# Optimization experiments

Hardware: AMD Instinct MI355X
Metric: run time of the kernel (lower is better)

## Reference

```python
import jax, jax.numpy as jnp
import numpy as np

S, B, D, H, L = 512, 1, 1024, 1024, 2  # seq, batch(=1 forced by view([1,-1])), input, hidden, layers


def _lstm_scan(xs, w_ih, w_hh, b, reverse=False):
    """Run an LSTMCell over xs [S,1,in]; returns (h_final, c_final, outs [S,1,H]).
    Torch LSTMCell gate order: i, f, g, o. b = b_ih + b_hh (combined)."""
    Hd = w_hh.shape[1]
    def step(carry, x):
        h, c = carry
        gates = x @ w_ih.T + h @ w_hh.T + b  # [1, 4H]
        i, f, g, o = jnp.split(gates, 4, axis=-1)
        c = jax.nn.sigmoid(f) * c + jax.nn.sigmoid(i) * jnp.tanh(g)
        h = jax.nn.sigmoid(o) * jnp.tanh(c)
        return (h, c), h
    init = (jnp.zeros((1, Hd), xs.dtype), jnp.zeros((1, Hd), xs.dtype))
    (h, c), outs = jax.lax.scan(step, init, xs, reverse=reverse)
    return h, c, outs


def setup_inputs() -> dict:
    key = jax.random.key(0)
    ks = jax.random.split(key, 13)
    sc = lambda fan_in: 1.0 / np.sqrt(fan_in)
    def W(k, rows, cols):
        return jax.random.uniform(k, (rows, cols), jnp.float32, -sc(cols), sc(cols))
    inp = {"x": jax.random.normal(ks[0], (S, B, D), jnp.float32)}
    # layer 0 (input D), fwd and bwd cells
    inp["w_ih0f"] = W(ks[1], 4 * H, D); inp["w_hh0f"] = W(ks[2], 4 * H, H)
    inp["b0f"] = jnp.zeros((4 * H,), jnp.float32)
    inp["w_ih0b"] = W(ks[3], 4 * H, D); inp["w_hh0b"] = W(ks[4], 4 * H, H)
    inp["b0b"] = jnp.zeros((4 * H,), jnp.float32)
    # layer 1 (input 2H from bidirectional concat)
    inp["w_ih1f"] = W(ks[5], 4 * H, 2 * H); inp["w_hh1f"] = W(ks[6], 4 * H, H)
    inp["b1f"] = jnp.zeros((4 * H,), jnp.float32)
    inp["w_ih1b"] = W(ks[7], 4 * H, 2 * H); inp["w_hh1b"] = W(ks[8], 4 * H, H)
    inp["b1b"] = jnp.zeros((4 * H,), jnp.float32)
    return inp


def reference(x, w_ih0f, w_hh0f, b0f, w_ih0b, w_hh0b, b0b,
              w_ih1f, w_hh1f, b1f, w_ih1b, w_hh1b, b1b):
    xs = x.reshape(x.shape[0], 1, -1)  # view([1,-1]) per step with batch=1
    # layer 0
    hf0, cf0, outs_f = _lstm_scan(xs, w_ih0f, w_hh0f, b0f, reverse=False)
    hb0, cb0, outs_b = _lstm_scan(xs, w_ih0b, w_hh0b, b0b, reverse=True)
    outs0 = jnp.concatenate([outs_f, outs_b], axis=-1)  # [S,1,2H]
    # layer 1 runs on layer-0 concat outputs; NOTE: due to a bug in the original
    # (output_sequence never reset), outputs_concat after layer 1 reuses layer-0
    # outputs, so the returned sequence is outs0, while layer-1 contributes only
    # its final hidden/cell states.
    hf1, cf1, _ = _lstm_scan(outs0, w_ih1f, w_hh1f, b1f, reverse=False)
    hb1, cb1, _ = _lstm_scan(outs0, w_ih1b, w_hh1b, b1b, reverse=True)
    final_h = jnp.stack([jnp.concatenate([hf0, hb0], axis=0),
                         jnp.concatenate([hf1, hb1], axis=0)])  # [L,2,H]
    final_c = jnp.stack([jnp.concatenate([cf0, cb0], axis=0),
                         jnp.concatenate([cf1, cb1], axis=0)])  # [L,2,H]
    return final_h, final_c, outs0
```

## Files before the change

### kernel.cpp

```cpp
#include <hip/hip_runtime.h>

#define SEQ 512
#define CAN 0x7FC0DEADu

__global__ __launch_bounds__(256) void gemm_bias2(
    const float* __restrict__ X,
    const float* __restrict__ Wf, const float* __restrict__ Wb,
    const float* __restrict__ biasf, const float* __restrict__ biasb,
    float* __restrict__ Gf, float* __restrict__ Gb,
    int M, int N, int K)
{
    const float* W    = blockIdx.z ? Wb : Wf;
    const float* bias = blockIdx.z ? biasb : biasf;
    float*       G    = blockIdx.z ? Gb : Gf;
    __shared__ float Xs[16][65];
    __shared__ float Ws[16][65];
    int tid = threadIdx.x;
    int tx = tid & 15, ty = tid >> 4;
    int m0 = blockIdx.y * 64, n0 = blockIdx.x * 64;
    float acc[4][4] = {};
    for (int k0 = 0; k0 < K; k0 += 16) {
        int row = tid >> 2, kq = (tid & 3) << 2;
        float4 vx = *(const float4*)(X + (size_t)(m0 + row) * K + k0 + kq);
        Xs[kq + 0][row] = vx.x; Xs[kq + 1][row] = vx.y;
        Xs[kq + 2][row] = vx.z; Xs[kq + 3][row] = vx.w;
        float4 vw = *(const float4*)(W + (size_t)(n0 + row) * K + k0 + kq);
        Ws[kq + 0][row] = vw.x; Ws[kq + 1][row] = vw.y;
        Ws[kq + 2][row] = vw.z; Ws[kq + 3][row] = vw.w;
        __syncthreads();
        #pragma unroll
        for (int k = 0; k < 16; ++k) {
            float a[4], b[4];
            #pragma unroll
            for (int i = 0; i < 4; ++i) a[i] = Xs[k][ty * 4 + i];
            #pragma unroll
            for (int j = 0; j < 4; ++j) b[j] = Ws[k][tx * 4 + j];
            #pragma unroll
            for (int i = 0; i < 4; ++i)
                #pragma unroll
                for (int j = 0; j < 4; ++j)
                    acc[i][j] = fmaf(a[i], b[j], acc[i][j]);
        }
        __syncthreads();
    }
    #pragma unroll
    for (int i = 0; i < 4; ++i) {
        int m = m0 + ty * 4 + i;
        #pragma unroll
        for (int j = 0; j < 4; ++j) {
            int n = n0 + tx * 4 + j;
            G[(size_t)m * N + n] = acc[i][j] + bias[n];
        }
    }
}

__global__ __launch_bounds__(256) void init_bufs(
    unsigned* __restrict__ flags, unsigned* __restrict__ hist_u,
    unsigned* __restrict__ h1_u)
{
    int i = blockIdx.x * 256 + threadIdx.x;
    if (i < 2048) flags[i] = 0u;
    int stride = gridDim.x * 256;
    for (int k = i; k < 512 * 2048; k += stride) {
        hist_u[k] = CAN;
        h1_u[k]   = CAN;
    }
}

__device__ __forceinline__ bool has_can(unsigned long long v) {
    return ((unsigned)v == CAN) | ((unsigned)(v >> 32) == CAN);
}

__global__ __launch_bounds__(256, 1) void lstm_recur(
    const float* __restrict__ Gf, const float* __restrict__ Gb,
    const float* __restrict__ Whf, const float* __restrict__ Whb,
    float* __restrict__ hist,
    float* __restrict__ h1buf,
    float* __restrict__ fin_h,
    float* __restrict__ fin_c,
    unsigned* __restrict__ flags,
    int layer)
{
    __shared__ float4 h4s[256];
    __shared__ float part[8 * 33];
    __shared__ float c_s[8];

    int tid = threadIdx.x;
    int cell = blockIdx.x >> 7;
    int gblk = blockIdx.x & 127;
    int j0 = gblk << 3;

    const float* Wh  = cell ? Whb : Whf;
    const float* Gin = cell ? Gb  : Gf;
    unsigned* myflags = flags + cell * 512;
    float* hout = (layer == 0) ? hist : h1buf;

    int tr = tid & 31, chunk = tid >> 5;
    int grow = ((tr >> 3) << 10) + j0 + (tr & 7);

    const float4* wrow = (const float4*)(Wh + (size_t)grow * 1024) + (chunk << 5);
    float4 w[32];
    #pragma unroll
    for (int i = 0; i < 32; ++i) w[i] = wrow[i];
    #pragma unroll
    for (int i = 0; i < 32; ++i)
        asm volatile("" : "+v"(w[i].x), "+v"(w[i].y), "+v"(w[i].z), "+v"(w[i].w));

    if (tid < 8) c_s[tid] = 0.f;

    for (int it = 0; it < SEQ; ++it) {
        int t = cell ? (SEQ - 1 - it) : it;

        float gpre = 0.f;
        if (tid < 32) gpre = Gin[(size_t)t * 4096 + grow];

        if (it == 0) {
            h4s[tid] = make_float4(0.f, 0.f, 0.f, 0.f);
        } else {
            if (tid < 64) {
                const unsigned* f0 = myflags + tid * 4;
                const unsigned* f1 = myflags + 256 + tid * 4;
                unsigned tgt = (unsigned)it;
                for (;;) {
                    unsigned a = __hip_atomic_load(f0, __ATOMIC_RELAXED,
                                                   __HIP_MEMORY_SCOPE_AGENT);
                    unsigned b = __hip_atomic_load(f1, __ATOMIC_RELAXED,
                                                   __HIP_MEMORY_SCOPE_AGENT);
                    if (__all(a >= tgt && b >= tgt)) break;
                    __builtin_amdgcn_s_sleep(1);
                }
            }
            __syncthreads();
            const float* hp;
            if (layer == 0)
                hp = cell ? (hist + (size_t)(t + 1) * 2048 + 1024)
                          : (hist + (size_t)(t - 1) * 2048);
            else
                hp = cell ? (h1buf + (size_t)(t + 1) * 2048 + 1024)
                          : (h1buf + (size_t)(t - 1) * 2048);
            const unsigned long long* hp64 = (const unsigned long long*)hp;
            unsigned long long u0, u1;
            for (;;) {
                u0 = __hip_atomic_load(hp64 + 2 * tid, __ATOMIC_RELAXED,
                                       __HIP_MEMORY_SCOPE_AGENT);
                u1 = __hip_atomic_load(hp64 + 2 * tid + 1, __ATOMIC_RELAXED,
                                       __HIP_MEMORY_SCOPE_AGENT);
                if (!(has_can(u0) | has_can(u1))) break;
            }
            h4s[tid] = make_float4(__uint_as_float((unsigned)u0),
                                   __uint_as_float((unsigned)(u0 >> 32)),
                                   __uint_as_float((unsigned)u1),
                                   __uint_as_float((unsigned)(u1 >> 32)));
        }
        __syncthreads();

        float a0 = 0.f, a1 = 0.f, a2 = 0.f, a3 = 0.f;
        const float4* hc = (const float4*)h4s + (chunk << 5);
        #pragma unroll
        for (int i = 0; i < 32; i += 4) {
            float4 h0 = hc[i], h1 = hc[i + 1], h2 = hc[i + 2], h3 = hc[i + 3];
            a0 = fmaf(w[i].x, h0.x, a0);     a0 = fmaf(w[i].y, h0.y, a0);
            a0 = fmaf(w[i].z, h0.z, a0);     a0 = fmaf(w[i].w, h0.w, a0);
            a1 = fmaf(w[i+1].x, h1.x, a1);   a1 = fmaf(w[i+1].y, h1.y, a1);
            a1 = fmaf(w[i+1].z, h1.z, a1);   a1 = fmaf(w[i+1].w, h1.w, a1);
            a2 = fmaf(w[i+2].x, h2.x, a2);   a2 = fmaf(w[i+2].y, h2.y, a2);
            a2 = fmaf(w[i+2].z, h2.z, a2);   a2 = fmaf(w[i+2].w, h2.w, a2);
            a3 = fmaf(w[i+3].x, h3.x, a3);   a3 = fmaf(w[i+3].y, h3.y, a3);
            a3 = fmaf(w[i+3].z, h3.z, a3);   a3 = fmaf(w[i+3].w, h3.w, a3);
        }
        part[chunk * 33 + tr] = (a0 + a1) + (a2 + a3);
        __syncthreads();

        if (tid < 32) {
            float v = gpre;
            #pragma unroll
            for (int k = 0; k < 8; ++k) v += part[k * 33 + tid];
            bool isg = (tid >> 3) == 2;
            float s = isg ? 2.f : 1.f;
            float e = __expf(-s * v);
            float r = 1.f / (1.f + e);
            float a = isg ? 2.f * r - 1.f : r;
            float si = __shfl(a, (tid & 7) + 0);
            float sf = __shfl(a, (tid & 7) + 8);
            float tg = __shfl(a, (tid & 7) + 16);
            float so = __shfl(a, (tid & 7) + 24);
            if (tid < 8) {
                float cnew = sf * c_s[tid] + si * tg;
                float e2 = __expf(-2.f * cnew);
                float hnew = so * (2.f / (1.f + e2) - 1.f);
                c_s[tid] = cnew;
                int j = j0 + tid;
                __hip_atomic_store(&hout[(size_t)t * 2048 + cell * 1024 + j], hnew,
                                   __ATOMIC_RELAXED, __HIP_MEMORY_SCOPE_AGENT);
                if (it == SEQ - 1) {
                    __hip_atomic_store(&fin_h[cell * 1024 + j], hnew,
                                       __ATOMIC_RELAXED, __HIP_MEMORY_SCOPE_AGENT);
                    __hip_atomic_store(&fin_c[cell * 1024 + j], cnew,
                                       __ATOMIC_RELAXED, __HIP_MEMORY_SCOPE_AGENT);
                }
            }
            if (tid == 0 && it < SEQ - 1) {
                __hip_atomic_store(&myflags[gblk * 4], (unsigned)(it + 1),
                                   __ATOMIC_RELAXED, __HIP_MEMORY_SCOPE_AGENT);
            }
        }
    }
}

extern "C" void kernel_launch(void* const* d_in, const int* in_sizes, int n_in,
                              void* d_out, int out_size, void* d_ws, size_t ws_size,
                              hipStream_t stream) {
    const float* x      = (const float*)d_in[0];
    const float* w_ih0f = (const float*)d_in[1];
    const float* w_hh0f = (const float*)d_in[2];
    const float* b0f    = (const float*)d_in[3];
    const float* w_ih0b = (const float*)d_in[4];
    const float* w_hh0b = (const float*)d_in[5];
    const float* b0b    = (const float*)d_in[6];
    const float* w_ih1f = (const float*)d_in[7];
    const float* w_hh1f = (const float*)d_in[8];
    const float* b1f    = (const float*)d_in[9];
    const float* w_ih1b = (const float*)d_in[10];
    const float* w_hh1b = (const float*)d_in[11];
    const float* b1b    = (const float*)d_in[12];

    float* out   = (float*)d_out;
    float* outs0 = out + 8192;
    float* ws    = (float*)d_ws;
    float* G0f   = ws;
    float* G0b   = ws + (size_t)512 * 4096;
    float* G1f   = ws;
    float* G1b   = ws + (size_t)512 * 4096;
    float* h1buf = ws + (size_t)2 * 512 * 4096;
    unsigned* flagbase = (unsigned*)(h1buf + (size_t)512 * 2048);
    unsigned* flags0 = flagbase;
    unsigned* flags1 = flagbase + 1024;

    hipLaunchKernelGGL(init_bufs, dim3(1024), dim3(256), 0, stream,
                       flagbase, (unsigned*)outs0, (unsigned*)h1buf);

    dim3 gb(64, 8, 2), tb(256);
    hipLaunchKernelGGL(gemm_bias2, gb, tb, 0, stream,
                       x, w_ih0f, w_ih0b, b0f, b0b, G0f, G0b, 512, 4096, 1024);

    {
        int layer = 0;
        const float* Gfp = G0f; const float* Gbp = G0b;
        const float* Whf = w_hh0f; const float* Whb = w_hh0b;
        float* hist = outs0; float* h1 = h1buf;
        float* finh = out;
        float* finc = out + 4096;
        unsigned* fl = flags0;
        void* args[] = {(void*)&Gfp, (void*)&Gbp, (void*)&Whf, (void*)&Whb,
                        (void*)&hist, (void*)&h1, (void*)&finh, (void*)&finc,
                        (void*)&fl, (void*)&layer};
        hipLaunchCooperativeKernel((void*)lstm_recur, dim3(256), dim3(256), args, 0, stream);
    }

    hipLaunchKernelGGL(gemm_bias2, gb, tb, 0, stream,
                       outs0, w_ih1f, w_ih1b, b1f, b1b, G1f, G1b, 512, 4096, 2048);

    {
        int layer = 1;
        const float* Gfp = G1f; const float* Gbp = G1b;
        const float* Whf = w_hh1f; const float* Whb = w_hh1b;
        float* hist = outs0; float* h1 = h1buf;
        float* finh = out + 2048;
        float* finc = out + 4096 + 2048;
        unsigned* fl = flags1;
        void* args[] = {(void*)&Gfp, (void*)&Gbp, (void*)&Whf, (void*)&Whb,
                        (void*)&hist, (void*)&h1, (void*)&finh, (void*)&finc,
                        (void*)&fl, (void*)&layer};
        hipLaunchCooperativeKernel((void*)lstm_recur, dim3(256), dim3(256), args, 0, stream);
    }
}
```

Baseline: 2.653 ms.

## Fuse input GEMMs and LSTM recurrences into one persistent cooperative kernel

Replaces the four separate launches (two input-projection GEMMs, two recurrent kernels) with one cooperative kernel of 512 blocks. The first 256 blocks run the layer-0 then layer-1 recurrences at raised priority. The other 256 blocks compute the input-projection GEMM tiles and publish per-row-chunk counters, so recurrence steps start as soon as their gate rows are ready. The layer-1 GEMM runs while layer 0 is still recurring, reusing the G0 buffers once layer-0 flags show those rows are consumed. This removes kernel boundaries and hides GEMM time behind the latency-bound recurrence, at the cost of sharing CUs between GEMM and recurrence blocks and adding spin-wait traffic.

```diff
diff --git a/kernel.cpp b/kernel.cpp
--- a/kernel.cpp
+++ b/kernel.cpp
@@ -2,6 +2,266 @@
 
 #define SEQ 512
 #define CAN 0x7FC0DEADu
+#define NRECUR 256
+#define NGEMM  256
+#define CNT_FULL 16384u
+
+#define LDA(p)   __hip_atomic_load((p), __ATOMIC_RELAXED, __HIP_MEMORY_SCOPE_AGENT)
+#define STA(p,v) __hip_atomic_store((p), (v), __ATOMIC_RELAXED, __HIP_MEMORY_SCOPE_AGENT)
+
+__device__ __forceinline__ bool has_can(unsigned long long v) {
+    return ((unsigned)v == CAN) | ((unsigned)(v >> 32) == CAN);
+}
+
+__global__ __launch_bounds__(256) void init_bufs(
+    unsigned* __restrict__ flags, unsigned* __restrict__ hist_u,
+    unsigned* __restrict__ h1_u)
+{
+    int i = blockIdx.x * 256 + threadIdx.x;
+    if (i < 2080) flags[i] = 0u;
+    int stride = gridDim.x * 256;
+    for (int k = i; k < 512 * 2048; k += stride) {
+        hist_u[k] = CAN;
+        h1_u[k]   = CAN;
+    }
+}
+
+template<bool XATOMIC>
+__device__ void gemm_tile(const float* __restrict__ X, const float* __restrict__ W,
+                          const float* __restrict__ bias, float* __restrict__ G,
+                          int m0, int n0, int K,
+                          float (*__restrict__ Xs)[65], float (*__restrict__ Ws)[65])
+{
+    int tid = threadIdx.x;
+    int tx = tid & 15, ty = tid >> 4;
+    int row = tid >> 2, kq = (tid & 3) << 2;
+    float acc[4][4] = {};
+    for (int k0 = 0; k0 < K; k0 += 16) {
+        float4 vx;
+        if (XATOMIC) {
+            const unsigned long long* xp =
+                (const unsigned long long*)(X + (size_t)(m0 + row) * K + k0 + kq);
+            unsigned long long u0, u1;
+            for (;;) {
+                u0 = LDA(xp); u1 = LDA(xp + 1);
+                if (!(has_can(u0) | has_can(u1))) break;
+            }
+            vx.x = __uint_as_float((unsigned)u0);
+            vx.y = __uint_as_float((unsigned)(u0 >> 32));
+            vx.z = __uint_as_float((unsigned)u1);
+            vx.w = __uint_as_float((unsigned)(u1 >> 32));
+        } else {
+            vx = *(const float4*)(X + (size_t)(m0 + row) * K + k0 + kq);
+        }
+        Xs[kq + 0][row] = vx.x; Xs[kq + 1][row] = vx.y;
+        Xs[kq + 2][row] = vx.z; Xs[kq + 3][row] = vx.w;
+        float4 vw = *(const float4*)(W + (size_t)(n0 + row) * K + k0 + kq);
+        Ws[kq + 0][row] = vw.x; Ws[kq + 1][row] = vw.y;
+        Ws[kq + 2][row] = vw.z; Ws[kq + 3][row] = vw.w;
+        __syncthreads();
+        #pragma unroll
+        for (int k = 0; k < 16; ++k) {
+            float a[4], b[4];
+            #pragma unroll
+            for (int i = 0; i < 4; ++i) a[i] = Xs[k][ty * 4 + i];
+            #pragma unroll
+            for (int j = 0; j < 4; ++j) b[j] = Ws[k][tx * 4 + j];
+            #pragma unroll
+            for (int i = 0; i < 4; ++i)
+                #pragma unroll
+                for (int j = 0; j < 4; ++j)
+                    acc[i][j] = fmaf(a[i], b[j], acc[i][j]);
+        }
+        __syncthreads();
+    }
+    #pragma unroll
+    for (int i = 0; i < 4; ++i) {
+        int m = m0 + ty * 4 + i;
+        #pragma unroll
+        for (int j = 0; j < 4; ++j) {
+            int n = n0 + tx * 4 + j;
+            STA(&G[(size_t)m * 4096 + n], acc[i][j] + bias[n]);
+        }
+    }
+}
+
+__device__ void wait_outs0(const unsigned* __restrict__ flags0, int rc)
+{
+    unsigned tf = (unsigned)(64 * rc + 64);
+    unsigned tb = (unsigned)(512 - 64 * rc);
+    int tid = threadIdx.x;
+    if (tid < 64) {
+        const unsigned* ff = flags0 + tid * 4;
+        const unsigned* fb = flags0 + 512 + tid * 4;
+        for (;;) {
+            unsigned a0 = LDA(ff), a1 = LDA(ff + 256);
+            unsigned b0 = LDA(fb), b1 = LDA(fb + 256);
+            if (__all(a0 >= tf && a1 >= tf && b0 >= tb && b1 >= tb)) break;
+            __builtin_amdgcn_s_sleep(32);
+        }
+    }
+    __syncthreads();
+}
+
+__device__ void recur_cell(
+    const float* __restrict__ Gin, const float* __restrict__ Wh,
+    float* __restrict__ hio, float* __restrict__ finh, float* __restrict__ finc,
+    unsigned* __restrict__ myflags, const unsigned* __restrict__ gcnt,
+    int cell, int gblk, float4* __restrict__ h4s, float* __restrict__ part)
+{
+    int tid = threadIdx.x;
+    int j0 = gblk << 3;
+    int tr = tid & 31, chunk = tid >> 5;
+    int grow = ((tr >> 3) << 10) + j0 + (tr & 7);
+
+    const float4* wrow = (const float4*)(Wh + (size_t)grow * 1024) + (chunk << 5);
+    float4 w[32];
+    #pragma unroll
+    for (int i = 0; i < 32; ++i) w[i] = wrow[i];
+    #pragma unroll
+    for (int i = 0; i < 32; ++i)
+        asm volatile("" : "+v"(w[i].x), "+v"(w[i].y), "+v"(w[i].z), "+v"(w[i].w));
+
+    float cprev = 0.f;
+
+    for (int it = 0; it < SEQ; ++it) {
+        int t = cell ? (SEQ - 1 - it) : it;
+
+        float gpre = 0.f;
+        if (tid < 32) {
+            const unsigned* cp = gcnt + (t >> 6);
+            while (LDA(cp) < CNT_FULL) __builtin_amdgcn_s_sleep(2);
+            gpre = __uint_as_float(LDA((const unsigned*)Gin + (size_t)t * 4096 + grow));
+        }
+
+        if (it == 0) {
+            h4s[tid] = make_float4(0.f, 0.f, 0.f, 0.f);
+        } else {
+            if (tid < 64) {
+                const unsigned* f0 = myflags + tid * 4;
+                const unsigned* f1 = myflags + 256 + tid * 4;
+                unsigned tgt = (unsigned)it;
+                for (;;) {
+                    unsigned a = LDA(f0);
+                    unsigned b = LDA(f1);
+                    if (__all(a >= tgt && b >= tgt)) break;
+                    __builtin_amdgcn_s_sleep(1);
+                }
+            }
+            __syncthreads();
+            const float* hp = cell ? (hio + (size_t)(t + 1) * 2048 + 1024)
+                                   : (hio + (size_t)(t - 1) * 2048);
+            const unsigned long long* hp64 = (const unsigned long long*)hp;
+            unsigned long long u0, u1;
+            for (;;) {
+                u0 = LDA(hp64 + 2 * tid);
+                u1 = LDA(hp64 + 2 * tid + 1);
+                if (!(has_can(u0) | has_can(u1))) break;
+            }
+            h4s[tid] = make_float4(__uint_as_float((unsigned)u0),
+                                   __uint_as_float((unsigned)(u0 >> 32)),
+                                   __uint_as_float((unsigned)u1),
+                                   __uint_as_float((unsigned)(u1 >> 32)));
+        }
+        __syncthreads();
+
+        float a0 = 0.f, a1 = 0.f, a2 = 0.f, a3 = 0.f;
+        const float4* hc = h4s + (chunk << 5);
+        #pragma unroll
+        for (int i = 0; i < 32; i += 4) {
+            float4 h0 = hc[i], h1 = hc[i + 1], h2 = hc[i + 2], h3 = hc[i + 3];
+            a0 = fmaf(w[i].x, h0.x, a0);     a0 = fmaf(w[i].y, h0.y, a0);
+            a0 = fmaf(w[i].z, h0.z, a0);     a0 = fmaf(w[i].w, h0.w, a0);
+            a1 = fmaf(w[i+1].x, h1.x, a1);   a1 = fmaf(w[i+1].y, h1.y, a1);
+            a1 = fmaf(w[i+1].z, h1.z, a1);   a1 = fmaf(w[i+1].w, h1.w, a1);
+            a2 = fmaf(w[i+2].x, h2.x, a2);   a2 = fmaf(w[i+2].y, h2.y, a2);
+            a2 = fmaf(w[i+2].z, h2.z, a2);   a2 = fmaf(w[i+2].w, h2.w, a2);
+            a3 = fmaf(w[i+3].x, h3.x, a3);   a3 = fmaf(w[i+3].y, h3.y, a3);
+            a3 = fmaf(w[i+3].z, h3.z, a3);   a3 = fmaf(w[i+3].w, h3.w, a3);
+        }
+        part[chunk * 33 + tr] = (a0 + a1) + (a2 + a3);
+        __syncthreads();
+
+        if (tid < 32) {
+            float v = gpre;
+            #pragma unroll
+            for (int k = 0; k < 8; ++k) v += part[k * 33 + tid];
+            bool isg = (tid >> 3) == 2;
+            float s = isg ? 2.f : 1.f;
+            float e = __expf(-s * v);
+            float r = 1.f / (1.f + e);
+            float a = isg ? 2.f * r - 1.f : r;
+            float si = __shfl(a, (tid & 7) + 0);
+            float sf = __shfl(a, (tid & 7) + 8);
+            float tg = __shfl(a, (tid & 7) + 16);
+            float so = __shfl(a, (tid & 7) + 24);
+            if (tid < 8) {
+                float cnew = sf * cprev + si * tg;
+                float e2 = __expf(-2.f * cnew);
+                float hnew = so * (2.f / (1.f + e2) - 1.f);
+                cprev = cnew;
+                int j = j0 + tid;
+                STA(&hio[(size_t)t * 2048 + cell * 1024 + j], hnew);
+                if (it == SEQ - 1) {
+                    STA(&finh[j], hnew);
+                    STA(&finc[j], cnew);
+                }
+            }
+            if (tid == 0)
+                STA(&myflags[gblk * 4], (unsigned)(it + 1));
+        }
+    }
+}
+
+__global__ __launch_bounds__(256, 2) void lstm_fused(
+    const float* __restrict__ x,
+    const float* __restrict__ w_ih0f, const float* __restrict__ w_hh0f, const float* __restrict__ b0f,
+    const float* __restrict__ w_ih0b, const float* __restrict__ w_hh0b, const float* __restrict__ b0b,
+    const float* __restrict__ w_ih1f, const float* __restrict__ w_hh1f, const float* __restrict__ b1f,
+    const float* __restrict__ w_ih1b, const float* __restrict__ w_hh1b, const float* __restrict__ b1b,
+    float* __restrict__ G0f, float* __restrict__ G0b,
+    float* __restrict__ hist, float* __restrict__ h1buf,
+    float* __restrict__ out,
+    unsigned* __restrict__ flags0, unsigned* __restrict__ flags1,
+    unsigned* __restrict__ g0cnt, unsigned* __restrict__ g1cnt)
+{
+    __shared__ float4 h4s[256];
+    __shared__ float part[8 * 33];
+    __shared__ float Xs[16][65];
+    __shared__ float Ws[16][65];
+
+    int bid = blockIdx.x;
+    if (bid < NRECUR) {
+        __builtin_amdgcn_s_setprio(1);
+        int cell = (bid >> 7) & 1;
+        int gblk = bid & 127;
+        recur_cell(cell ? G0b : G0f, cell ? w_hh0b : w_hh0f, hist,
+                   out + cell * 1024, out + 4096 + cell * 1024,
+                   flags0 + cell * 512, g0cnt + cell * 8, cell, gblk, h4s, part);
+        recur_cell(cell ? G0b : G0f, cell ? w_hh1b : w_hh1f, h1buf,
+                   out + 2048 + cell * 1024, out + 4096 + 2048 + cell * 1024,
+                   flags1 + cell * 512, g1cnt + cell * 8, cell, gblk, h4s, part);
+    } else {
+        int gid = bid - NRECUR;
+        for (int idx = gid; idx < 1024; idx += NGEMM) {
+            int k = idx >> 7, half = (idx >> 6) & 1, cc = idx & 63;
+            int rc = half ? (7 - k) : k;
+            gemm_tile<false>(x, half ? w_ih0b : w_ih0f, half ? b0b : b0f,
+                             half ? G0b : G0f, rc * 64, cc * 64, 1024, Xs, Ws);
+            __hip_atomic_fetch_add(&g0cnt[half * 8 + rc], 1u,
+                                   __ATOMIC_RELEASE, __HIP_MEMORY_SCOPE_AGENT);
+        }
+        for (int idx = gid; idx < 1024; idx += NGEMM) {
+            int k = idx >> 7, half = (idx >> 6) & 1, cc = idx & 63;
+            int rc = half ? (7 - k) : k;
+            wait_outs0(flags0, rc);
+            gemm_tile<true>(hist, half ? w_ih1b : w_ih1f, half ? b1b : b1f,
+                            half ? G0b : G0f, rc * 64, cc * 64, 2048, Xs, Ws);
+            __hip_atomic_fetch_add(&g1cnt[half * 8 + rc], 1u,
+                                   __ATOMIC_RELEASE, __HIP_MEMORY_SCOPE_AGENT);
+        }
+    }
+}
 
 __global__ __launch_bounds__(256) void gemm_bias2(
     const float* __restrict__ X,
@@ -54,32 +314,12 @@
     }
 }
 
-__global__ __launch_bounds__(256) void init_bufs(
-    unsigned* __restrict__ flags, unsigned* __restrict__ hist_u,
-    unsigned* __restrict__ h1_u)
-{
-    int i = blockIdx.x * 256 + threadIdx.x;
-    if (i < 2048) flags[i] = 0u;
-    int stride = gridDim.x * 256;
-    for (int k = i; k < 512 * 2048; k += stride) {
-        hist_u[k] = CAN;
-        h1_u[k]   = CAN;
-    }
-}
-
-__device__ __forceinline__ bool has_can(unsigned long long v) {
-    return ((unsigned)v == CAN) | ((unsigned)(v >> 32) == CAN);
-}
-
 __global__ __launch_bounds__(256, 1) void lstm_recur(
     const float* __restrict__ Gf, const float* __restrict__ Gb,
     const float* __restrict__ Whf, const float* __restrict__ Whb,
-    float* __restrict__ hist,
-    float* __restrict__ h1buf,
-    float* __restrict__ fin_h,
-    float* __restrict__ fin_c,
-    unsigned* __restrict__ flags,
-    int layer)
+    float* __restrict__ hist, float* __restrict__ h1buf,
+    float* __restrict__ fin_h, float* __restrict__ fin_c,
+    unsigned* __restrict__ flags, int layer)
 {
     __shared__ float4 h4s[256];
     __shared__ float part[8 * 33];
@@ -110,7 +350,6 @@
 
     for (int it = 0; it < SEQ; ++it) {
         int t = cell ? (SEQ - 1 - it) : it;
-
         float gpre = 0.f;
         if (tid < 32) gpre = Gin[(size_t)t * 4096 + grow];
 
@@ -122,10 +361,8 @@
                 const unsigned* f1 = myflags + 256 + tid * 4;
                 unsigned tgt = (unsigned)it;
                 for (;;) {
-                    unsigned a = __hip_atomic_load(f0, __ATOMIC_RELAXED,
-                                                   __HIP_MEMORY_SCOPE_AGENT);
-                    unsigned b = __hip_atomic_load(f1, __ATOMIC_RELAXED,
-                                                   __HIP_MEMORY_SCOPE_AGENT);
+                    unsigned a = LDA(f0);
+                    unsigned b = LDA(f1);
                     if (__all(a >= tgt && b >= tgt)) break;
                     __builtin_amdgcn_s_sleep(1);
                 }
@@ -141,10 +378,8 @@
             const unsigned long long* hp64 = (const unsigned long long*)hp;
             unsigned long long u0, u1;
             for (;;) {
-                u0 = __hip_atomic_load(hp64 + 2 * tid, __ATOMIC_RELAXED,
-                                       __HIP_MEMORY_SCOPE_AGENT);
-                u1 = __hip_atomic_load(hp64 + 2 * tid + 1, __ATOMIC_RELAXED,
-                                       __HIP_MEMORY_SCOPE_AGENT);
+                u0 = LDA(hp64 + 2 * tid);
+                u1 = LDA(hp64 + 2 * tid + 1);
                 if (!(has_can(u0) | has_can(u1))) break;
             }
             h4s[tid] = make_float4(__uint_as_float((unsigned)u0),
@@ -155,7 +390,7 @@
         __syncthreads();
 
         float a0 = 0.f, a1 = 0.f, a2 = 0.f, a3 = 0.f;
-        const float4* hc = (const float4*)h4s + (chunk << 5);
+        const float4* hc = h4s + (chunk << 5);
         #pragma unroll
         for (int i = 0; i < 32; i += 4) {
             float4 h0 = hc[i], h1 = hc[i + 1], h2 = hc[i + 2], h3 = hc[i + 3];
@@ -190,19 +425,14 @@
                 float hnew = so * (2.f / (1.f + e2) - 1.f);
                 c_s[tid] = cnew;
                 int j = j0 + tid;
-                __hip_atomic_store(&hout[(size_t)t * 2048 + cell * 1024 + j], hnew,
-                                   __ATOMIC_RELAXED, __HIP_MEMORY_SCOPE_AGENT);
+                STA(&hout[(size_t)t * 2048 + cell * 1024 + j], hnew);
                 if (it == SEQ - 1) {
-                    __hip_atomic_store(&fin_h[cell * 1024 + j], hnew,
-                                       __ATOMIC_RELAXED, __HIP_MEMORY_SCOPE_AGENT);
-                    __hip_atomic_store(&fin_c[cell * 1024 + j], cnew,
-                                       __ATOMIC_RELAXED, __HIP_MEMORY_SCOPE_AGENT);
+                    STA(&fin_h[cell * 1024 + j], hnew);
+                    STA(&fin_c[cell * 1024 + j], cnew);
                 }
             }
-            if (tid == 0 && it < SEQ - 1) {
-                __hip_atomic_store(&myflags[gblk * 4], (unsigned)(it + 1),
-                                   __ATOMIC_RELAXED, __HIP_MEMORY_SCOPE_AGENT);
-            }
+            if (tid == 0 && it < SEQ - 1)
+                STA(&myflags[gblk * 4], (unsigned)(it + 1));
         }
     }
 }
@@ -229,48 +459,72 @@
     float* ws    = (float*)d_ws;
     float* G0f   = ws;
     float* G0b   = ws + (size_t)512 * 4096;
-    float* G1f   = ws;
-    float* G1b   = ws + (size_t)512 * 4096;
     float* h1buf = ws + (size_t)2 * 512 * 4096;
     unsigned* flagbase = (unsigned*)(h1buf + (size_t)512 * 2048);
     unsigned* flags0 = flagbase;
     unsigned* flags1 = flagbase + 1024;
+    unsigned* g0cnt  = flagbase + 2048;
+    unsigned* g1cnt  = flagbase + 2064;
 
     hipLaunchKernelGGL(init_bufs, dim3(1024), dim3(256), 0, stream,
                        flagbase, (unsigned*)outs0, (unsigned*)h1buf);
 
-    dim3 gb(64, 8, 2), tb(256);
-    hipLaunchKernelGGL(gemm_bias2, gb, tb, 0, stream,
-                       x, w_ih0f, w_ih0b, b0f, b0b, G0f, G0b, 512, 4096, 1024);
-
-    {
-        int layer = 0;
-        const float* Gfp = G0f; const float* Gbp = G0b;
-        const float* Whf = w_hh0f; const float* Whb = w_hh0b;
-        float* hist = outs0; float* h1 = h1buf;
-        float* finh = out;
-        float* finc = out + 4096;
-        unsigned* fl = flags0;
-        void* args[] = {(void*)&Gfp, (void*)&Gbp, (void*)&Whf, (void*)&Whb,
-                        (void*)&hist, (void*)&h1, (void*)&finh, (void*)&finc,
-                        (void*)&fl, (void*)&layer};
-        hipLaunchCooperativeKernel((void*)lstm_recur, dim3(256), dim3(256), args, 0, stream);
-    }
-
-    hipLaunchKernelGGL(gemm_bias2, gb, tb, 0, stream,
-                       outs0, w_ih1f, w_ih1b, b1f, b1b, G1f, G1b, 512, 4096, 2048);
-
-    {
-        int layer = 1;
-        const float* Gfp = G1f; const float* Gbp = G1b;
-        const float* Whf = w_hh1f; const float* Whb = w_hh1b;
-        float* hist = outs0; float* h1 = h1buf;
-        float* finh = out + 2048;
-        float* finc = out + 4096 + 2048;
-        unsigned* fl = flags1;
-        void* args[] = {(void*)&Gfp, (void*)&Gbp, (void*)&Whf, (void*)&Whb,
-                        (void*)&hist, (void*)&h1, (void*)&finh, (void*)&finc,
-                        (void*)&fl, (void*)&layer};
-        hipLaunchCooperativeKernel((void*)lstm_recur, dim3(256), dim3(256), args, 0, stream);
-    }
-}
+    int occ = 0;
+    hipOccupancyMaxActiveBlocksPerMultiprocessor(&occ, lstm_fused, 256, 0);
+
+    if (occ >= 2) {
+        const float* xp = x;
+        const float* a1 = w_ih0f; const float* a2 = w_hh0f; const float* a3 = b0f;
+        const float* a4 = w_ih0b; const float* a5 = w_hh0b; const float* a6 = b0b;
+        const float* a7 = w_ih1f; const float* a8 = w_hh1f; const float* a9 = b1f;
+        const float* aa = w_ih1b; const float* ab = w_hh1b; const float* ac = b1b;
+        float* g0fp = G0f; float* g0bp = G0b;
+        float* histp = outs0; float* h1p = h1buf; float* outp = out;
+        unsigned* f0p = flags0; unsigned* f1p = flags1;
+        unsigned* c0p = g0cnt;  unsigned* c1p = g1cnt;
+        void* args[] = {(void*)&xp,
+                        (void*)&a1, (void*)&a2, (void*)&a3,
+                        (void*)&a4, (void*)&a5, (void*)&a6,
+                        (void*)&a7, (void*)&a8, (void*)&a9,
+                        (void*)&aa, (void*)&ab, (void*)&ac,
+                        (void*)&g0fp, (void*)&g0bp,
+                        (void*)&histp, (void*)&h1p, (void*)&outp,
+                        (void*)&f0p, (void*)&f1p, (void*)&c0p, (void*)&c1p};
+        hipLaunchCooperativeKernel((void*)lstm_fused, dim3(NRECUR + NGEMM),
+                                   dim3(256), args, 0, stream);
+    } else {
+        float* G1f = ws;
+        float* G1b = ws + (size_t)512 * 4096;
+        dim3 gb(64, 8, 2), tb(256);
+        hipLaunchKernelGGL(gemm_bias2, gb, tb, 0, stream,
+                           x, w_ih0f, w_ih0b, b0f, b0b, G0f, G0b, 512, 4096, 1024);
+        {
+            int layer = 0;
+            const float* Gfp = G0f; const float* Gbp = G0b;
+            const float* Whf = w_hh0f; const float* Whb = w_hh0b;
+            float* hist = outs0; float* h1 = h1buf;
+            float* finh = out;
+            float* finc = out + 4096;
+            unsigned* fl = flags0;
+            void* args[] = {(void*)&Gfp, (void*)&Gbp, (void*)&Whf, (void*)&Whb,
+                            (void*)&hist, (void*)&h1, (void*)&finh, (void*)&finc,
+                            (void*)&fl, (void*)&layer};
+            hipLaunchCooperativeKernel((void*)lstm_recur, dim3(256), dim3(256), args, 0, stream);
+        }
+        hipLaunchKernelGGL(gemm_bias2, gb, tb, 0, stream,
+                           outs0, w_ih1f, w_ih1b, b1f, b1b, G1f, G1b, 512, 4096, 2048);
+        {
+            int layer = 1;
+            const float* Gfp = G1f; const float* Gbp = G1b;
+            const float* Whf = w_hh1f; const float* Whb = w_hh1b;
+            float* hist = outs0; float* h1 = h1buf;
+            float* finh = out + 2048;
+            float* finc = out + 4096 + 2048;
+            unsigned* fl = flags1;
+            void* args[] = {(void*)&Gfp, (void*)&Gbp, (void*)&Whf, (void*)&Whb,
+                            (void*)&hist, (void*)&h1, (void*)&finh, (void*)&finc,
+                            (void*)&fl, (void*)&layer};
+            hipLaunchCooperativeKernel((void*)lstm_recur, dim3(256), dim3(256), args, 0, stream);
+        }
+    }
+}
```

Result: no change. 2.656 ms (+0.1%).
